# Optimization experiments

Measured on AMD Instinct MI355X. Metric: run time of the kernel, lower is better.

Reference implementation:

```python
import jax, jax.numpy as jnp
import numpy as np

N_NODES = 50000
N_EDGES = 800000
F_IN = 128
HIDDEN = 32
HEADS = 4
F_OUT = 64
NEG_SLOPE = 0.2


def setup_inputs() -> dict:
    key = jax.random.key(0)
    ks = jax.random.split(key, 9)
    x = jax.random.normal(ks[0], (N_NODES, F_IN), dtype=jnp.float32)
    edge_index = jax.random.randint(ks[1], (2, N_EDGES), 0, N_NODES, dtype=jnp.int64)
    edge_weight = jax.random.uniform(ks[2], (N_EDGES,), dtype=jnp.float32)
    # GATConv parameters
    W = jax.random.normal(ks[3], (F_IN, HEADS * HIDDEN), dtype=jnp.float32) * (1.0 / np.sqrt(F_IN))
    a_src = jax.random.normal(ks[4], (HEADS, HIDDEN), dtype=jnp.float32) * 0.1
    a_dst = jax.random.normal(ks[5], (HEADS, HIDDEN), dtype=jnp.float32) * 0.1
    bias = jnp.zeros((HEADS * HIDDEN,), dtype=jnp.float32)
    # output linear
    W2 = jax.random.normal(ks[6], (HEADS * HIDDEN, F_OUT), dtype=jnp.float32) * (1.0 / np.sqrt(HEADS * HIDDEN))
    b2 = jnp.zeros((F_OUT,), dtype=jnp.float32)
    return {"x": x, "edge_index": edge_index, "edge_weight": edge_weight,
            "W": W, "a_src": a_src, "a_dst": a_dst, "bias": bias,
            "W2": W2, "b2": b2}


def reference(x, edge_index, edge_weight, W, a_src, a_dst, bias, W2, b2):
    src, dst = edge_index[0], edge_index[1]
    # linear transform per head: [N, H, C]
    h = (x @ W).reshape(-1, HEADS, HIDDEN)
    # per-node attention logits: [N, H]
    alpha_s = jnp.einsum('nhc,hc->nh', h, a_src)
    alpha_d = jnp.einsum('nhc,hc->nh', h, a_dst)
    # per-edge scores: [E, H]
    e = alpha_s[src] + alpha_d[dst]
    e = jnp.where(e >= 0, e, NEG_SLOPE * e)  # LeakyReLU(0.2)
    # segment softmax over destination neighborhoods
    m = jax.ops.segment_max(e, dst, num_segments=N_NODES)  # [N, H]
    ex = jnp.exp(e - m[dst])
    denom = jax.ops.segment_sum(ex, dst, num_segments=N_NODES)  # [N, H]
    alpha = ex / (denom[dst] + 1e-16)  # [E, H]
    # weighted scatter-add aggregation: [N, H, C]
    msgs = alpha[:, :, None] * h[src]
    out = jax.ops.segment_sum(msgs, dst, num_segments=N_NODES)
    out = out.reshape(-1, HEADS * HIDDEN) + bias
    out = jax.nn.elu(out)
    return out @ W2 + b2
```

## Files before the change

### kernel.cpp

```cpp
#include <hip/hip_runtime.h>

#define N_NODES 50000
#define N_EDGES 800000
#define F_IN 128
#define HH 128
#define HEADS 4
#define HIDDEN 32
#define F_OUT 64
#define NEG_SLOPE 0.2f
#define CAP 64

#define NODE_BLOCKS ((N_NODES + 31) / 32)
#define FILL_BLOCKS ((N_EDGES / 4 + 255) / 256)

typedef __attribute__((ext_vector_type(8))) short short8v;
typedef __attribute__((ext_vector_type(4))) float float4v;

__device__ __forceinline__ unsigned short f2bf(float f) {
    unsigned int u = __float_as_uint(f);
    u = (u + 0x7FFFu + ((u >> 16) & 1u)) >> 16;
    return (unsigned short)u;
}

__global__ __launch_bounds__(256) void k_node_fill(
    const float* __restrict__ x, const float* __restrict__ W,
    const float* __restrict__ a_src, const float* __restrict__ a_dst,
    unsigned short* __restrict__ h_bf,
    float* __restrict__ as_out, float* __restrict__ ad_out,
    const int* __restrict__ ei, int* __restrict__ cursor, int* __restrict__ bucket)
{
    __shared__ __align__(16) unsigned short xs[32][136];

    if (blockIdx.x >= NODE_BLOCKS) {
        int e0 = ((blockIdx.x - NODE_BLOCKS) * 256 + threadIdx.x) * 4;
        if (e0 < N_EDGES) {
            int4 s4 = *(const int4*)&ei[e0];
            int4 d4 = *(const int4*)&ei[N_EDGES + e0];
            bucket[(size_t)d4.x * CAP + (atomicAdd(&cursor[d4.x], 1) & (CAP - 1))] = s4.x;
            bucket[(size_t)d4.y * CAP + (atomicAdd(&cursor[d4.y], 1) & (CAP - 1))] = s4.y;
            bucket[(size_t)d4.z * CAP + (atomicAdd(&cursor[d4.z], 1) & (CAP - 1))] = s4.z;
            bucket[(size_t)d4.w * CAP + (atomicAdd(&cursor[d4.w], 1) & (CAP - 1))] = s4.w;
        }
        return;
    }

    const int tid  = threadIdx.x;
    const int base = blockIdx.x * 32;

    for (int i = tid; i < 32 * 32; i += 256) {
        int r = i >> 5, c4 = i & 31;
        int n = base + r;
        float4 v = (n < N_NODES) ? *(const float4*)&x[(size_t)n * F_IN + c4 * 4]
                                 : make_float4(0.f, 0.f, 0.f, 0.f);
        ushort4 hv;
        hv.x = f2bf(v.x); hv.y = f2bf(v.y); hv.z = f2bf(v.z); hv.w = f2bf(v.w);
        *(ushort4*)&xs[r][c4 * 4] = hv;
    }
    __syncthreads();

    const int w    = tid >> 6;
    const int lane = tid & 63;
    const int l15  = lane & 15;
    const int l4   = lane >> 4;

    short8v bfrag[4][2];
    #pragma unroll
    for (int ks = 0; ks < 4; ++ks) {
        #pragma unroll
        for (int nn = 0; nn < 2; ++nn) {
            int c  = w * 32 + nn * 16 + l15;
            int kb = ks * 32 + l4 * 8;
            short8v b;
            #pragma unroll
            for (int j = 0; j < 8; ++j)
                b[j] = (short)f2bf(W[(kb + j) * HH + c]);
            bfrag[ks][nn] = b;
        }
    }

    float4v acc[2][2] = {};
    #pragma unroll
    for (int ks = 0; ks < 4; ++ks) {
        short8v a0 = *(const short8v*)&xs[l15][ks * 32 + l4 * 8];
        short8v a1 = *(const short8v*)&xs[16 + l15][ks * 32 + l4 * 8];
        acc[0][0] = __builtin_amdgcn_mfma_f32_16x16x32_bf16(a0, bfrag[ks][0], acc[0][0], 0, 0, 0);
        acc[0][1] = __builtin_amdgcn_mfma_f32_16x16x32_bf16(a0, bfrag[ks][1], acc[0][1], 0, 0, 0);
        acc[1][0] = __builtin_amdgcn_mfma_f32_16x16x32_bf16(a1, bfrag[ks][0], acc[1][0], 0, 0, 0);
        acc[1][1] = __builtin_amdgcn_mfma_f32_16x16x32_bf16(a1, bfrag[ks][1], acc[1][1], 0, 0, 0);
    }

    const float as0 = a_src[w * 32 + l15],      ad0 = a_dst[w * 32 + l15];
    const float as1 = a_src[w * 32 + 16 + l15], ad1 = a_dst[w * 32 + 16 + l15];

    #pragma unroll
    for (int m = 0; m < 2; ++m) {
        #pragma unroll
        for (int reg = 0; reg < 4; ++reg) {
            int node = base + m * 16 + l4 * 4 + reg;
            float v0 = acc[m][0][reg];
            float v1 = acc[m][1][reg];
            if (node < N_NODES) {
                h_bf[(size_t)node * HH + w * 32 + l15]      = f2bf(v0);
                h_bf[(size_t)node * HH + w * 32 + 16 + l15] = f2bf(v1);
            }
            float ps = v0 * as0 + v1 * as1;
            float pd = v0 * ad0 + v1 * ad1;
            #pragma unroll
            for (int off = 1; off < 16; off <<= 1) {
                ps += __shfl_xor(ps, off, 16);
                pd += __shfl_xor(pd, off, 16);
            }
            if (l15 == 0 && node < N_NODES) {
                as_out[node * HEADS + w] = ps;
                ad_out[node * HEADS + w] = pd;
            }
        }
    }
}

__global__ __launch_bounds__(256) void k_gather(
    const int* __restrict__ cnt_arr, const int* __restrict__ bucket,
    const float* __restrict__ as_, const float* __restrict__ ad_,
    const unsigned short* __restrict__ h_bf, float* __restrict__ agg)
{
    int gid = blockIdx.x * 256 + threadIdx.x;
    int n = gid >> 6;
    if (n >= N_NODES) return;
    const int lane = gid & 63;
    const int hd  = lane >> 4;
    const int e16 = lane & 15;

    const float advv = ad_[n * 4 + hd];
    const int cnt = cnt_arr[n];
    const int* brow = &bucket[(size_t)n * CAP];

    float accx = 0.f, accy = 0.f, sum = 0.f;

    for (int cb = 0; cb < cnt; cb += 16) {
        int m = cnt - cb; if (m > 16) m = 16;
        int s = 0; float exown = 0.f;
        if (e16 < m) {
            s = brow[cb + e16];
            float lg = as_[s * 4 + hd] + advv;
            lg = lg >= 0.f ? lg : NEG_SLOPE * lg;
            exown = __expf(lg);
        }

#define GAT_BODY(j)                                                            \
        {                                                                      \
            float al = __shfl(exown, (hd << 4) + (j));                         \
            int   sj = __shfl(s,     (hd << 4) + (j));                         \
            unsigned int hv = *(const unsigned int*)&h_bf[(size_t)sj * HH + lane * 2]; \
            sum += al;                                                         \
            accx = fmaf(al, __uint_as_float((hv & 0xFFFFu) << 16), accx);      \
            accy = fmaf(al, __uint_as_float(hv & 0xFFFF0000u), accy);          \
        }

        if (m == 16) {
            #pragma unroll
            for (int j = 0; j < 16; ++j) GAT_BODY(j)
        } else {
            for (int j = 0; j < m; ++j) GAT_BODY(j)
        }
#undef GAT_BODY
    }

    float inv = 1.f / (sum + 1e-16f);
    *(float2*)&agg[(size_t)n * HH + lane * 2] = make_float2(accx * inv, accy * inv);
}

__global__ __launch_bounds__(256) void k_output(
    const float* __restrict__ agg, const float* __restrict__ bias,
    const float* __restrict__ W2, const float* __restrict__ b2,
    float* __restrict__ out)
{
    __shared__ float eb[64][132];

    const int tid  = threadIdx.x;
    const int base = blockIdx.x * 64;

    for (int i = tid; i < 64 * 32; i += 256) {
        int r = i >> 5, c4 = i & 31;
        int n = base + r;
        float4 v = (n < N_NODES) ? *(const float4*)&agg[(size_t)n * HH + c4 * 4]
                                 : make_float4(0.f, 0.f, 0.f, 0.f);
        float4 b = *(const float4*)&bias[c4 * 4];
        v.x += b.x; v.y += b.y; v.z += b.z; v.w += b.w;
        v.x = v.x > 0.f ? v.x : __expf(v.x) - 1.f;
        v.y = v.y > 0.f ? v.y : __expf(v.y) - 1.f;
        v.z = v.z > 0.f ? v.z : __expf(v.z) - 1.f;
        v.w = v.w > 0.f ? v.w : __expf(v.w) - 1.f;
        *(float4*)&eb[r][c4 * 4] = v;
    }
    __syncthreads();

    const int cg = tid & 15;
    const int q  = tid >> 4;

    float4 b2v = *(const float4*)&b2[cg * 4];
    float4 acc[4] = { b2v, b2v, b2v, b2v };
    for (int k4 = 0; k4 < 32; ++k4) {
        const float* wr = &W2[(k4 * 4) * F_OUT + cg * 4];
        float4 w0 = *(const float4*)(wr);
        float4 w1 = *(const float4*)(wr + F_OUT);
        float4 w2 = *(const float4*)(wr + 2 * F_OUT);
        float4 w3 = *(const float4*)(wr + 3 * F_OUT);
        #pragma unroll
        for (int j = 0; j < 4; ++j) {
            float4 xv = *(const float4*)&eb[q * 4 + j][k4 * 4];
            acc[j].x = fmaf(xv.x, w0.x, acc[j].x); acc[j].y = fmaf(xv.x, w0.y, acc[j].y);
            acc[j].z = fmaf(xv.x, w0.z, acc[j].z); acc[j].w = fmaf(xv.x, w0.w, acc[j].w);
            acc[j].x = fmaf(xv.y, w1.x, acc[j].x); acc[j].y = fmaf(xv.y, w1.y, acc[j].y);
            acc[j].z = fmaf(xv.y, w1.z, acc[j].z); acc[j].w = fmaf(xv.y, w1.w, acc[j].w);
            acc[j].x = fmaf(xv.z, w2.x, acc[j].x); acc[j].y = fmaf(xv.z, w2.y, acc[j].y);
            acc[j].z = fmaf(xv.z, w2.z, acc[j].z); acc[j].w = fmaf(xv.z, w2.w, acc[j].w);
            acc[j].x = fmaf(xv.w, w3.x, acc[j].x); acc[j].y = fmaf(xv.w, w3.y, acc[j].y);
            acc[j].z = fmaf(xv.w, w3.z, acc[j].z); acc[j].w = fmaf(xv.w, w3.w, acc[j].w);
        }
    }
    #pragma unroll
    for (int j = 0; j < 4; ++j) {
        int n = base + q * 4 + j;
        if (n < N_NODES)
            *(float4*)&out[(size_t)n * F_OUT + cg * 4] = acc[j];
    }
}

extern "C" void kernel_launch(void* const* d_in, const int* in_sizes, int n_in,
                              void* d_out, int out_size, void* d_ws, size_t ws_size,
                              hipStream_t stream)
{
    const float* x     = (const float*)d_in[0];
    const int*   ei    = (const int*)  d_in[1];
    const float* W     = (const float*)d_in[3];
    const float* a_src = (const float*)d_in[4];
    const float* a_dst = (const float*)d_in[5];
    const float* bias  = (const float*)d_in[6];
    const float* W2    = (const float*)d_in[7];
    const float* b2    = (const float*)d_in[8];
    float* out = (float*)d_out;

    char* ws = (char*)d_ws;
    unsigned short* h_bf = (unsigned short*)ws;
    float* as_   = (float*)(ws + (size_t)N_NODES * HH * 2);
    float* ad_   = as_ + (size_t)N_NODES * HEADS;
    int*   cursor= (int*)(ad_ + (size_t)N_NODES * HEADS);
    int*   bucket= cursor + N_NODES;
    float* agg   = (float*)(bucket + (size_t)N_NODES * CAP);

    hipMemsetAsync(cursor, 0, (size_t)N_NODES * sizeof(int), stream);

    k_node_fill<<<NODE_BLOCKS + FILL_BLOCKS, 256, 0, stream>>>(
        x, W, a_src, a_dst, h_bf, as_, ad_, ei, cursor, bucket);
    k_gather<<<(N_NODES * 64 + 255) / 256, 256, 0, stream>>>(cursor, bucket, as_, ad_, h_bf, agg);
    k_output<<<(N_NODES + 63) / 64, 256, 0, stream>>>(agg, bias, W2, b2, out);
}
```

Before: 133.2 us.

## Prepack bf16 weight fragments and fold attention vectors into W for MFMA logits

Adds a single-block prep kernel that converts W to bf16 once, already laid out in the per-lane MFMA B-fragment order. The same kernel precomputes W·a_src and W·a_dst per head, packed as an extra 16-wide fragment. The node kernel then loads fragments with vector loads instead of doing strided fp32 loads and conversions in every block. It gets the per-node attention logits from two extra MFMAs instead of multiply plus 16-lane shuffle reductions. The cost is an additional serialized kernel launch. The logits are now computed from bf16-rounded folded weights rather than from fp32 h, which changes numerics slightly.

```diff
diff --git a/kernel.cpp b/kernel.cpp
--- a/kernel.cpp
+++ b/kernel.cpp
@@ -22,9 +22,63 @@
     return (unsigned short)u;
 }
 
+__global__ __launch_bounds__(256) void k_prep(
+    const float* __restrict__ W, const float* __restrict__ a_src,
+    const float* __restrict__ a_dst,
+    unsigned short* __restrict__ Wf, unsigned short* __restrict__ Waf)
+{
+    __shared__ float Wl[F_IN * HH];
+    __shared__ float Wa[F_IN][8];
+
+    const int t = threadIdx.x;
+    for (int i = t; i < F_IN * HH / 4; i += 256)
+        *(float4*)&Wl[i * 4] = *(const float4*)&W[i * 4];
+    __syncthreads();
+
+    if (t < F_IN) {
+        const float* wr = &Wl[t * HH];
+        #pragma unroll
+        for (int hd = 0; hd < 4; ++hd) {
+            float ss = 0.f, dd = 0.f;
+            #pragma unroll
+            for (int c = 0; c < 32; ++c) {
+                float wv = wr[hd * 32 + c];
+                ss = fmaf(wv, a_src[hd * 32 + c], ss);
+                dd = fmaf(wv, a_dst[hd * 32 + c], dd);
+            }
+            Wa[t][hd] = ss; Wa[t][4 + hd] = dd;
+        }
+    }
+    __syncthreads();
+
+    const int w = t >> 6, lane = t & 63, l15 = lane & 15, l4 = lane >> 4;
+
+    #pragma unroll
+    for (int ks = 0; ks < 4; ++ks) {
+        #pragma unroll
+        for (int nn = 0; nn < 2; ++nn) {
+            short8v b;
+            #pragma unroll
+            for (int j = 0; j < 8; ++j)
+                b[j] = (short)f2bf(Wl[(ks * 32 + l4 * 8 + j) * HH + w * 32 + nn * 16 + l15]);
+            *(short8v*)&Wf[(size_t)((ks * 2 + nn) * 256 + t) * 8] = b;
+        }
+    }
+    if (t < 64) {
+        #pragma unroll
+        for (int ks = 0; ks < 4; ++ks) {
+            short8v b;
+            #pragma unroll
+            for (int j = 0; j < 8; ++j)
+                b[j] = (l15 < 8) ? (short)f2bf(Wa[ks * 32 + l4 * 8 + j][l15]) : (short)0;
+            *(short8v*)&Waf[(size_t)(ks * 64 + lane) * 8] = b;
+        }
+    }
+}
+
 __global__ __launch_bounds__(256) void k_node_fill(
-    const float* __restrict__ x, const float* __restrict__ W,
-    const float* __restrict__ a_src, const float* __restrict__ a_dst,
+    const float* __restrict__ x,
+    const unsigned short* __restrict__ Wf, const unsigned short* __restrict__ Waf,
     unsigned short* __restrict__ h_bf,
     float* __restrict__ as_out, float* __restrict__ ad_out,
     const int* __restrict__ ei, int* __restrict__ cursor, int* __restrict__ bucket)
@@ -63,22 +117,16 @@
     const int l15  = lane & 15;
     const int l4   = lane >> 4;
 
-    short8v bfrag[4][2];
+    short8v bfrag[4][2], wafrag[4];
     #pragma unroll
     for (int ks = 0; ks < 4; ++ks) {
-        #pragma unroll
-        for (int nn = 0; nn < 2; ++nn) {
-            int c  = w * 32 + nn * 16 + l15;
-            int kb = ks * 32 + l4 * 8;
-            short8v b;
-            #pragma unroll
-            for (int j = 0; j < 8; ++j)
-                b[j] = (short)f2bf(W[(kb + j) * HH + c]);
-            bfrag[ks][nn] = b;
-        }
+        bfrag[ks][0] = *(const short8v*)&Wf[(size_t)((ks * 2 + 0) * 256 + tid) * 8];
+        bfrag[ks][1] = *(const short8v*)&Wf[(size_t)((ks * 2 + 1) * 256 + tid) * 8];
+        wafrag[ks]   = *(const short8v*)&Waf[(size_t)(ks * 64 + lane) * 8];
     }
 
     float4v acc[2][2] = {};
+    float4v accL[2] = {};
     #pragma unroll
     for (int ks = 0; ks < 4; ++ks) {
         short8v a0 = *(const short8v*)&xs[l15][ks * 32 + l4 * 8];
@@ -87,32 +135,22 @@
         acc[0][1] = __builtin_amdgcn_mfma_f32_16x16x32_bf16(a0, bfrag[ks][1], acc[0][1], 0, 0, 0);
         acc[1][0] = __builtin_amdgcn_mfma_f32_16x16x32_bf16(a1, bfrag[ks][0], acc[1][0], 0, 0, 0);
         acc[1][1] = __builtin_amdgcn_mfma_f32_16x16x32_bf16(a1, bfrag[ks][1], acc[1][1], 0, 0, 0);
-    }
-
-    const float as0 = a_src[w * 32 + l15],      ad0 = a_dst[w * 32 + l15];
-    const float as1 = a_src[w * 32 + 16 + l15], ad1 = a_dst[w * 32 + 16 + l15];
+        accL[0]   = __builtin_amdgcn_mfma_f32_16x16x32_bf16(a0, wafrag[ks], accL[0], 0, 0, 0);
+        accL[1]   = __builtin_amdgcn_mfma_f32_16x16x32_bf16(a1, wafrag[ks], accL[1], 0, 0, 0);
+    }
 
     #pragma unroll
     for (int m = 0; m < 2; ++m) {
         #pragma unroll
         for (int reg = 0; reg < 4; ++reg) {
             int node = base + m * 16 + l4 * 4 + reg;
-            float v0 = acc[m][0][reg];
-            float v1 = acc[m][1][reg];
-            if (node < N_NODES) {
-                h_bf[(size_t)node * HH + w * 32 + l15]      = f2bf(v0);
-                h_bf[(size_t)node * HH + w * 32 + 16 + l15] = f2bf(v1);
-            }
-            float ps = v0 * as0 + v1 * as1;
-            float pd = v0 * ad0 + v1 * ad1;
-            #pragma unroll
-            for (int off = 1; off < 16; off <<= 1) {
-                ps += __shfl_xor(ps, off, 16);
-                pd += __shfl_xor(pd, off, 16);
-            }
-            if (l15 == 0 && node < N_NODES) {
-                as_out[node * HEADS + w] = ps;
-                ad_out[node * HEADS + w] = pd;
+            if (node >= N_NODES) continue;
+            h_bf[(size_t)node * HH + w * 32 + l15]      = f2bf(acc[m][0][reg]);
+            h_bf[(size_t)node * HH + w * 32 + 16 + l15] = f2bf(acc[m][1][reg]);
+            if (w == 0 && l15 < 8) {
+                float lg = accL[m][reg];
+                if (l15 < 4) as_out[node * HEADS + l15]       = lg;
+                else         ad_out[node * HEADS + (l15 - 4)] = lg;
             }
         }
     }
@@ -241,8 +279,10 @@
     float* out = (float*)d_out;
 
     char* ws = (char*)d_ws;
-    unsigned short* h_bf = (unsigned short*)ws;
-    float* as_   = (float*)(ws + (size_t)N_NODES * HH * 2);
+    unsigned short* Wf   = (unsigned short*)ws;
+    unsigned short* Waf  = Wf + 8 * 256 * 8;
+    unsigned short* h_bf = Waf + 4 * 64 * 8;
+    float* as_   = (float*)(h_bf + (size_t)N_NODES * HH);
     float* ad_   = as_ + (size_t)N_NODES * HEADS;
     int*   cursor= (int*)(ad_ + (size_t)N_NODES * HEADS);
     int*   bucket= cursor + N_NODES;
@@ -250,8 +290,9 @@
 
     hipMemsetAsync(cursor, 0, (size_t)N_NODES * sizeof(int), stream);
 
+    k_prep<<<1, 256, 0, stream>>>(W, a_src, a_dst, Wf, Waf);
     k_node_fill<<<NODE_BLOCKS + FILL_BLOCKS, 256, 0, stream>>>(
-        x, W, a_src, a_dst, h_bf, as_, ad_, ei, cursor, bucket);
+        x, Wf, Waf, h_bf, as_, ad_, ei, cursor, bucket);
     k_gather<<<(N_NODES * 64 + 255) / 256, 256, 0, stream>>>(cursor, bucket, as_, ad_, h_bf, agg);
     k_output<<<(N_NODES + 63) / 64, 256, 0, stream>>>(agg, bias, W2, b2, out);
 }
```

Result: slower. 138.0 us (+3.6%).
